# Kernel tuning notes

Measured on AMD Instinct MI355X. Metric: run time of the kernel, lower is better.

The kernel has to match this reference:

```python
import jax, jax.numpy as jnp
import numpy as np

B, S, D, H, E = 4, 1024, 1024, 16, 4
HD = D // H
FF = 4 * D
EPS = 1e-5


def _ln(x):
    # normalize only; per-expert affine applied by caller
    mu = jnp.mean(x, axis=-1, keepdims=True)
    var = jnp.mean(jnp.square(x - mu), axis=-1, keepdims=True)
    return (x - mu) * jax.lax.rsqrt(var + EPS)


def setup_inputs() -> dict:
    key = jax.random.key(0)
    ks = jax.random.split(key, 12)
    s = 0.02
    inp = {
        "x": jax.random.normal(ks[0], (B, S, D), jnp.float32),
        # attention router
        "Wr_a": jax.random.normal(ks[1], (D, E), jnp.float32) * s,
        "br_a": jnp.zeros((E,), jnp.float32),
        # per-expert attention params
        "g_a": jnp.ones((E, D), jnp.float32),
        "b_a": jnp.zeros((E, D), jnp.float32),
        "Wqkv": jax.random.normal(ks[2], (E, D, 3 * D), jnp.float32) * s,
        "bqkv": jnp.zeros((E, 3 * D), jnp.float32),
        "Wpr": jax.random.normal(ks[3], (E, D, D), jnp.float32) * s,
        "bpr": jnp.zeros((E, D), jnp.float32),
        # MLP router
        "Wr_m": jax.random.normal(ks[4], (D, E), jnp.float32) * s,
        "br_m": jnp.zeros((E,), jnp.float32),
        # per-expert MLP params
        "g_m": jnp.ones((E, D), jnp.float32),
        "b_m": jnp.zeros((E, D), jnp.float32),
        "Wfc": jax.random.normal(ks[5], (E, D, FF), jnp.float32) * s,
        "bfc": jnp.zeros((E, FF), jnp.float32),
        "Wp2": jax.random.normal(ks[6], (E, FF, D), jnp.float32) * s,
        "bp2": jnp.zeros((E, D), jnp.float32),
    }
    return inp


def _block(x, Wr_a, br_a, g_a, b_a, Wqkv, bqkv, Wpr, bpr,
           Wr_m, br_m, g_m, b_m, Wfc, bfc, Wp2, bp2):
    N = B * S
    h = x.reshape(N, D)

    # ---- MoT attention (routing_all_possible_path: dense score-weighted mix) ----
    score = jax.nn.softmax(h @ Wr_a + br_a, axis=-1)          # [N,E]
    hn = _ln(h)                                                # shared normalization
    hln = hn[None, :, :] * g_a[:, None, :] + b_a[:, None, :]  # [E,N,D]
    qkv_e = jnp.einsum('end,edf->enf', hln, Wqkv) + bqkv[:, None, :]  # [E,N,3D]
    qkv = jnp.einsum('ne,enf->nf', score, qkv_e)               # [N,3D]

    q, k, v = jnp.split(qkv.reshape(B, S, 3 * D), 3, axis=-1)
    q = q.reshape(B, S, H, HD).transpose(0, 2, 1, 3)           # [B,H,S,hd]
    k = k.reshape(B, S, H, HD).transpose(0, 2, 1, 3)
    v = v.reshape(B, S, H, HD).transpose(0, 2, 1, 3)

    aw = jnp.einsum('bhqd,bhkd->bhqk', q, k) / jnp.sqrt(jnp.float32(HD))
    causal = jnp.tril(jnp.ones((S, S), bool))
    aw = jnp.where(causal, aw, jnp.finfo(aw.dtype).min)
    p = jax.nn.softmax(aw, axis=-1)
    a = jnp.einsum('bhqk,bhkd->bhqd', p, v)                    # [B,H,S,hd]
    a = a.transpose(0, 2, 1, 3).reshape(N, D)

    attn_out = jnp.einsum('ne,nd,edf->nf', score, a, Wpr) + score @ bpr
    y = x + attn_out.reshape(B, S, D)

    # ---- MoT MLP (same dense routed-expert pattern) ----
    h2 = y.reshape(N, D)
    score2 = jax.nn.softmax(h2 @ Wr_m + br_m, axis=-1)         # [N,E]
    hn2 = _ln(h2)
    hln2 = hn2[None, :, :] * g_m[:, None, :] + b_m[:, None, :]  # [E,N,D]
    inter = jax.nn.gelu(jnp.einsum('end,edf->enf', hln2, Wfc) + bfc[:, None, :])  # [E,N,FF]
    mlp_out = jnp.einsum('ne,enf,efd->nd', score2, inter, Wp2) + score2 @ bp2
    return y + mlp_out.reshape(B, S, D)


def reference(x, Wr_a, br_a, g_a, b_a, Wqkv, bqkv, Wpr, bpr,
              Wr_m, br_m, g_m, b_m, Wfc, bfc, Wp2, bp2):
    return _block(x, Wr_a, br_a, g_a, b_a, Wqkv, bqkv, Wpr, bpr,
                  Wr_m, br_m, g_m, b_m, Wfc, bfc, Wp2, bp2)
```

## Files before the change

kernel.cpp:

```cpp
#include <hip/hip_runtime.h>
#include <hip/hip_bf16.h>

typedef __bf16 bf16x8 __attribute__((ext_vector_type(8)));
typedef float f32x4 __attribute__((ext_vector_type(4)));
typedef unsigned short u16;
typedef u16 u16x8 __attribute__((ext_vector_type(8)));
typedef u16 u16x4 __attribute__((ext_vector_type(4)));

#define B_ 4
#define S_ 1024
#define D_ 1024
#define E_ 4
#define H_ 16
#define FF_ 4096
#define N_ 4096

__device__ __forceinline__ u16 f2bf(float f) {
  __hip_bfloat16 h = __float2bfloat16(f);
  return *reinterpret_cast<u16*>(&h);
}
__device__ __forceinline__ float bf2f(u16 v) {
  return __uint_as_float(((unsigned)v) << 16);
}

#define BAR()                         \
  {                                   \
    asm volatile("" ::: "memory");    \
    __builtin_amdgcn_s_barrier();     \
    asm volatile("" ::: "memory");    \
  }

__global__ __launch_bounds__(256) void tcvt(const float* __restrict__ src,
                                            u16* __restrict__ dst, int R, int C) {
  __shared__ float t[32][33];
  long base = (long)blockIdx.z * R * C;
  src += base; dst += base;
  int r0 = blockIdx.y * 32, c0 = blockIdx.x * 32;
  int tx = threadIdx.x, ty = threadIdx.y;
#pragma unroll
  for (int i = 0; i < 4; i++)
    t[ty + i * 8][tx] = src[(long)(r0 + ty + i * 8) * C + c0 + tx];
  __syncthreads();
#pragma unroll
  for (int i = 0; i < 4; i++)
    dst[(long)(c0 + ty + i * 8) * R + r0 + tx] = f2bf(t[tx][ty + i * 8]);
}

template <int YMODE>
__global__ __launch_bounds__(256) void ln_router_expand(
    const float* __restrict__ X, const float* __restrict__ Wr, const float* __restrict__ br,
    const float* __restrict__ g, const float* __restrict__ bb,
    float* __restrict__ score_out, u16* __restrict__ Aout,
    long stride_e, long stride_n, int scale_flag,
    const float* __restrict__ score_a, const float* __restrict__ bpr,
    const u16* __restrict__ prt, float* __restrict__ ybuf) {
  int n = blockIdx.x, t = threadIdx.x;
  int lane = t & 63, wave = t >> 6;
  int d0 = t * 4;
  const float* xr = X + (long)n * D_;
  float4 xv = *reinterpret_cast<const float4*>(&xr[d0]);
  if (YMODE) {
    float4 sa4 = reinterpret_cast<const float4*>(score_a)[n];
    float sw[4] = {sa4.x, sa4.y, sa4.z, sa4.w};
    float4 b0 = *reinterpret_cast<const float4*>(&bpr[d0]);
    float4 b1 = *reinterpret_cast<const float4*>(&bpr[D_ + d0]);
    float4 b2 = *reinterpret_cast<const float4*>(&bpr[2 * D_ + d0]);
    float4 b3 = *reinterpret_cast<const float4*>(&bpr[3 * D_ + d0]);
    xv.x += sa4.x * b0.x + sa4.y * b1.x + sa4.z * b2.x + sa4.w * b3.x;
    xv.y += sa4.x * b0.y + sa4.y * b1.y + sa4.z * b2.y + sa4.w * b3.y;
    xv.z += sa4.x * b0.z + sa4.y * b1.z + sa4.z * b2.z + sa4.w * b3.z;
    xv.w += sa4.x * b0.w + sa4.y * b1.w + sa4.z * b2.w + sa4.w * b3.w;
    long idx = (long)n * D_ + d0;
#pragma unroll
    for (int zz = 0; zz < 4; zz++) {
      u16x4 pv = *reinterpret_cast<const u16x4*>(&prt[(long)zz * 4194304 + idx]);
      xv.x += sw[zz] * bf2f(pv[0]); xv.y += sw[zz] * bf2f(pv[1]);
      xv.z += sw[zz] * bf2f(pv[2]); xv.w += sw[zz] * bf2f(pv[3]);
    }
    *reinterpret_cast<float4*>(&ybuf[idx]) = xv;
  }
  float vals[6];
  vals[0] = xv.x + xv.y + xv.z + xv.w;
  vals[1] = xv.x * xv.x + xv.y * xv.y + xv.z * xv.z + xv.w * xv.w;
  {
    float4 w0 = reinterpret_cast<const float4*>(Wr)[d0];
    float4 w1 = reinterpret_cast<const float4*>(Wr)[d0 + 1];
    float4 w2 = reinterpret_cast<const float4*>(Wr)[d0 + 2];
    float4 w3 = reinterpret_cast<const float4*>(Wr)[d0 + 3];
    vals[2] = xv.x * w0.x + xv.y * w1.x + xv.z * w2.x + xv.w * w3.x;
    vals[3] = xv.x * w0.y + xv.y * w1.y + xv.z * w2.y + xv.w * w3.y;
    vals[4] = xv.x * w0.z + xv.y * w1.z + xv.z * w2.z + xv.w * w3.z;
    vals[5] = xv.x * w0.w + xv.y * w1.w + xv.z * w2.w + xv.w * w3.w;
  }
#pragma unroll
  for (int o = 1; o < 64; o <<= 1) {
#pragma unroll
    for (int j = 0; j < 6; j++) vals[j] += __shfl_xor(vals[j], o, 64);
  }
  __shared__ float red[4][6];
  if (lane == 0) {
#pragma unroll
    for (int j = 0; j < 6; j++) red[wave][j] = vals[j];
  }
  __syncthreads();
  float tot[6];
#pragma unroll
  for (int j = 0; j < 6; j++) tot[j] = red[0][j] + red[1][j] + red[2][j] + red[3][j];
  float mean = tot[0] * (1.0f / D_);
  float var = tot[1] * (1.0f / D_) - mean * mean;
  float rstd = rsqrtf(var + 1e-5f);
  float lg0 = tot[2] + br[0], lg1 = tot[3] + br[1], lg2 = tot[4] + br[2], lg3 = tot[5] + br[3];
  float mx = fmaxf(fmaxf(lg0, lg1), fmaxf(lg2, lg3));
  float e0 = __expf(lg0 - mx), e1 = __expf(lg1 - mx), e2 = __expf(lg2 - mx), e3 = __expf(lg3 - mx);
  float inv = 1.0f / (e0 + e1 + e2 + e3);
  float sc[4] = {e0 * inv, e1 * inv, e2 * inv, e3 * inv};
  if (t == 0) {
    float4 s4 = make_float4(sc[0], sc[1], sc[2], sc[3]);
    *reinterpret_cast<float4*>(&score_out[(long)n * 4]) = s4;
  }
  float4 hn;
  hn.x = (xv.x - mean) * rstd; hn.y = (xv.y - mean) * rstd;
  hn.z = (xv.z - mean) * rstd; hn.w = (xv.w - mean) * rstd;
#pragma unroll
  for (int e = 0; e < 4; e++) {
    float4 ge = *reinterpret_cast<const float4*>(&g[e * D_ + d0]);
    float4 be = *reinterpret_cast<const float4*>(&bb[e * D_ + d0]);
    float s = scale_flag ? sc[e] : 1.0f;
    u16x4 o;
    o[0] = f2bf((hn.x * ge.x + be.x) * s);
    o[1] = f2bf((hn.y * ge.y + be.y) * s);
    o[2] = f2bf((hn.z * ge.z + be.z) * s);
    o[3] = f2bf((hn.w * ge.w + be.w) * s);
    *reinterpret_cast<u16x4*>(&Aout[(long)e * stride_e + (long)n * stride_n + d0]) = o;
  }
}

template <int MODE>
__global__ __launch_bounds__(512, 2) void g8(
    const u16* __restrict__ A, const u16* __restrict__ Bt, int K, int N, int kslice,
    const float* __restrict__ score, const float* __restrict__ bias,
    u16* __restrict__ outb, int eidx, long zstride, long bz) {
  __shared__ __align__(16) u16 lds0[65536];
  const int tid = threadIdx.x;
  const int w = tid >> 6, lane = tid & 63;
  const int l15 = lane & 15, l4 = lane >> 4;
  const int wr = w >> 2, wc = w & 3;

  const int gx = gridDim.x, gy = gridDim.y;
  const int total = gx * gy * gridDim.z;
  const int flat = blockIdx.x + gx * (blockIdx.y + gy * blockIdx.z);
  const int cpx = total >> 3;
  const int nf = (flat & 7) * cpx + (flat >> 3);
  const int bxi = nf % gx;
  const int tmp = nf / gx;
  const int byi = tmp % gy;
  const int z = tmp / gy;

  const long bm = (long)byi * 256, bn = (long)bxi * 256;
  const long k0 = bz ? 0L : (long)z * kslice;
  const u16* Btz = bz ? (Bt + (long)z * bz) : Bt;
  const int nt = kslice >> 6;

  const int cp = lane & 3;
  const int sr0 = w * 32 + (lane >> 2);
  const int sr1 = sr0 + 16;
  const int cl0 = cp ^ ((sr0 >> 1) & 3);
  const int cl1 = cp ^ ((sr1 >> 1) & 3);
  const u16* gA0 = A + (bm + sr0) * (long)K + k0 + cl0 * 8;
  const u16* gA1 = A + (bm + sr1) * (long)K + k0 + cl1 * 8;
  const u16* gB0 = Btz + (bn + sr0) * (long)K + k0 + cl0 * 8;
  const u16* gB1 = Btz + (bn + sr1) * (long)K + k0 + cl1 * 8;
  const int e0 = w * 1024;
  const int e1 = w * 1024 + 512;

  const int chA = l4 ^ ((l15 >> 1) & 3);
  const int rdA = (wr * 128 + l15) * 32 + chA * 8;
  const int rdB = (wc * 64 + l15) * 32 + chA * 8;

#define GLD(gsrc, ldsoff)                                                              \
  __builtin_amdgcn_global_load_lds(                                                    \
      (const __attribute__((address_space(1))) void*)(gsrc),                           \
      (__attribute__((address_space(3))) void*)(lds0 + (ldsoff)), 16, 0, 0)

  GLD(gA0, 0 + e0);
  GLD(gA1, 0 + e1);
  GLD(gB0, 16384 + e0);
  GLD(gB1, 16384 + e1);
  GLD(gA0 + 32, 8192 + e0);
  GLD(gA1 + 32, 8192 + e1);
  GLD(gB0 + 32, 24576 + e0);
  GLD(gB1 + 32, 24576 + e1);
  if (nt > 1) {
    GLD(gA0 + 64, 32768 + e0);
    GLD(gA1 + 64, 32768 + e1);
    GLD(gB0 + 64, 32768 + 16384 + e0);
    GLD(gB1 + 64, 32768 + 16384 + e1);
    GLD(gA0 + 96, 32768 + 8192 + e0);
    GLD(gA1 + 96, 32768 + 8192 + e1);
    GLD(gB0 + 96, 32768 + 24576 + e0);
    GLD(gB1 + 96, 32768 + 24576 + e1);
    asm volatile("s_waitcnt vmcnt(8)" ::: "memory");
  } else {
    asm volatile("s_waitcnt vmcnt(0)" ::: "memory");
  }
  BAR();

  f32x4 acc[8][4] = {};
  bf16x8 aC[8], bC[4], aN[8], bN[4];

#pragma unroll
  for (int i = 0; i < 8; i++) aC[i] = *(const bf16x8*)(lds0 + rdA + i * 512);
#pragma unroll
  for (int i = 0; i < 4; i++) bC[i] = *(const bf16x8*)(lds0 + 16384 + rdB + i * 512);

  for (int t = 0; t < nt; ++t) {
    const int base = (t & 1) * 32768;
    const int nb = base ^ 32768;
    const long ko2 = (long)(t + 2) * 64;
#pragma unroll
    for (int i = 0; i < 8; i++) aN[i] = *(const bf16x8*)(lds0 + base + 8192 + rdA + i * 512);
#pragma unroll
    for (int i = 0; i < 4; i++) bN[i] = *(const bf16x8*)(lds0 + base + 24576 + rdB + i * 512);
    if (t + 2 < nt) {
      GLD(gA0 + ko2, base + e0);
      GLD(gA1 + ko2, base + e1);
      GLD(gB0 + ko2, base + 16384 + e0);
      GLD(gB1 + ko2, base + 16384 + e1);
    }
    __builtin_amdgcn_sched_barrier(0);
    __builtin_amdgcn_s_setprio(1);
#pragma unroll
    for (int mi = 0; mi < 8; mi++)
#pragma unroll
      for (int ni = 0; ni < 4; ni++)
        acc[mi][ni] = __builtin_amdgcn_mfma_f32_16x16x32_bf16(aC[mi], bC[ni], acc[mi][ni], 0, 0, 0);
    __builtin_amdgcn_s_setprio(0);
    asm volatile("s_waitcnt lgkmcnt(0)" ::: "memory");
    if (t + 1 < nt) {
      if (t + 2 < nt) {
        asm volatile("s_waitcnt vmcnt(8)" ::: "memory");
      } else {
        asm volatile("s_waitcnt vmcnt(4)" ::: "memory");
      }
    }
    BAR();
    if (t + 1 < nt) {
#pragma unroll
      for (int i = 0; i < 8; i++) aC[i] = *(const bf16x8*)(lds0 + nb + rdA + i * 512);
#pragma unroll
      for (int i = 0; i < 4; i++) bC[i] = *(const bf16x8*)(lds0 + nb + 16384 + rdB + i * 512);
    }
    if (t + 2 < nt) {
      GLD(gA0 + ko2 + 32, base + 8192 + e0);
      GLD(gA1 + ko2 + 32, base + 8192 + e1);
      GLD(gB0 + ko2 + 32, base + 24576 + e0);
      GLD(gB1 + ko2 + 32, base + 24576 + e1);
    }
    __builtin_amdgcn_sched_barrier(0);
    __builtin_amdgcn_s_setprio(1);
#pragma unroll
    for (int mi = 0; mi < 8; mi++)
#pragma unroll
      for (int ni = 0; ni < 4; ni++)
        acc[mi][ni] = __builtin_amdgcn_mfma_f32_16x16x32_bf16(aN[mi], bN[ni], acc[mi][ni], 0, 0, 0);
    __builtin_amdgcn_s_setprio(0);
    asm volatile("s_waitcnt lgkmcnt(0)" ::: "memory");
    if (t + 1 < nt) {
      if (t + 2 < nt) {
        asm volatile("s_waitcnt vmcnt(8)" ::: "memory");
      } else {
        asm volatile("s_waitcnt vmcnt(0)" ::: "memory");
      }
    }
    BAR();
  }
#undef GLD

  const long zoff = (long)z * zstride;
#pragma unroll
  for (int ni = 0; ni < 4; ni++) {
    long col = bn + wc * 64 + ni * 16 + l15;
    float b4[4];
    float bcol = 0.0f;
    if (MODE == 0) {
#pragma unroll
      for (int e = 0; e < 4; e++) b4[e] = bias[(long)e * N + col];
    } else if (MODE == 2) {
      bcol = bias[col];
    }
#pragma unroll
    for (int mi = 0; mi < 8; mi++) {
#pragma unroll
      for (int r = 0; r < 4; r++) {
        long row = bm + wr * 128 + mi * 16 + l4 * 4 + r;
        float v = acc[mi][ni][r];
        if (MODE == 0) {
          float4 s4 = reinterpret_cast<const float4*>(score)[row];
          v += s4.x * b4[0] + s4.y * b4[1] + s4.z * b4[2] + s4.w * b4[3];
          outb[row * (long)N + col] = f2bf(v);
        } else if (MODE == 2) {
          float u = v + bcol;
          float zz = 0.7978845608f * (u + 0.044715f * u * u * u);
          float tt = __expf(2.0f * zz);
          float gel = u * (1.0f - 1.0f / (tt + 1.0f));
          outb[row * (long)N + col] = f2bf(gel * score[row * 4 + eidx]);
        } else {
          outb[zoff + row * (long)N + col] = f2bf(v);
        }
      }
    }
  }
}

__global__ __launch_bounds__(256) void attn_kernel(const u16* __restrict__ qkv,
                                                   u16* __restrict__ aout) {
  __shared__ __align__(16) u16 Kt[32 * 64];
  __shared__ __align__(16) u16 VT[64 * 32];
  __shared__ __align__(16) u16 Pl[4][16 * 32];
  int tid = threadIdx.x, wave = tid >> 6, lane = tid & 63;
  int l15 = lane & 15, l4 = lane >> 4;
  int qblk = blockIdx.x, bh = blockIdx.y;
  int b = bh >> 4, h = bh & 15;
  int q0 = qblk * 64 + wave * 16;
  const long LD = 3072;

  bf16x8 qf[2];
  {
    const u16* qp = qkv + (long)(b * 1024 + q0 + l15) * LD + h * 64 + l4 * 8;
    qf[0] = *(const bf16x8*)qp;
    qf[1] = *(const bf16x8*)(qp + 32);
  }
  f32x4 acc[4] = {};
  float m_run = -1e30f, l_run = 0.0f;
  int kv_end = qblk * 64 + 64;

  for (int kv0 = 0; kv0 < kv_end; kv0 += 32) {
    {
      int r = tid >> 3, c = (tid & 7) * 8;
      const u16* kp = qkv + (long)(b * 1024 + kv0 + r) * LD + 1024 + h * 64 + c;
      *(u16x8*)&Kt[r * 64 + c] = *(const u16x8*)kp;
      u16x8 vv = *(const u16x8*)(kp + 1024);
#pragma unroll
      for (int j = 0; j < 8; j++) VT[(c + j) * 32 + r] = vv[j];
    }
    __syncthreads();
    if (kv0 < q0 + 16) {
      float p[8];
      float pmax = -1e30f;
      int qg = q0 + l15;
#pragma unroll
      for (int ks = 0; ks < 2; ks++) {
        f32x4 st = {};
#pragma unroll
        for (int kc = 0; kc < 2; kc++) {
          bf16x8 kf = *(const bf16x8*)&Kt[(ks * 16 + l15) * 64 + kc * 32 + l4 * 8];
          st = __builtin_amdgcn_mfma_f32_16x16x32_bf16(kf, qf[kc], st, 0, 0, 0);
        }
#pragma unroll
        for (int r = 0; r < 4; r++) {
          int kvg = kv0 + ks * 16 + l4 * 4 + r;
          float v = st[r] * 0.125f;
          if (kvg > qg) v = -1e30f;
          p[ks * 4 + r] = v;
          pmax = fmaxf(pmax, v);
        }
      }
      pmax = fmaxf(pmax, __shfl_xor(pmax, 16, 64));
      pmax = fmaxf(pmax, __shfl_xor(pmax, 32, 64));
      float m_new = fmaxf(m_run, pmax);
      float alpha = __expf(m_run - m_new);
      float rsum = 0.f;
#pragma unroll
      for (int i = 0; i < 8; i++) {
        p[i] = __expf(p[i] - m_new);
        rsum += p[i];
      }
      rsum += __shfl_xor(rsum, 16, 64);
      rsum += __shfl_xor(rsum, 32, 64);
      l_run = l_run * alpha + rsum;
      m_run = m_new;
      float af4[4];
#pragma unroll
      for (int r = 0; r < 4; r++) af4[r] = __shfl(alpha, l4 * 4 + r, 64);
#pragma unroll
      for (int i = 0; i < 4; i++) {
#pragma unroll
        for (int r = 0; r < 4; r++) acc[i][r] *= af4[r];
      }
      u16* pw = &Pl[wave][0];
#pragma unroll
      for (int i = 0; i < 8; i++) {
        int ks = i >> 2, r = i & 3;
        pw[l15 * 32 + ks * 16 + l4 * 4 + r] = f2bf(p[i]);
      }
      bf16x8 pa = *(const bf16x8*)&pw[l15 * 32 + l4 * 8];
#pragma unroll
      for (int i = 0; i < 4; i++) {
        bf16x8 vf = *(const bf16x8*)&VT[(i * 16 + l15) * 32 + l4 * 8];
        acc[i] = __builtin_amdgcn_mfma_f32_16x16x32_bf16(pa, vf, acc[i], 0, 0, 0);
      }
    }
    __syncthreads();
  }

  float linv[4];
#pragma unroll
  for (int r = 0; r < 4; r++) {
    float lv = __shfl(l_run, l4 * 4 + r, 64);
    linv[r] = 1.0f / lv;
  }
#pragma unroll
  for (int r = 0; r < 4; r++) {
    int q = l4 * 4 + r;
    long nrow = (long)b * 1024 + q0 + q;
#pragma unroll
    for (int i = 0; i < 4; i++) {
      int d = h * 64 + i * 16 + l15;
      aout[nrow * 1024 + d] = f2bf(acc[i][r] * linv[r]);
    }
  }
}

template <int FIRST>
__global__ __launch_bounds__(256) void accum_out(const float* __restrict__ ybuf,
                                                 const float* __restrict__ score_m,
                                                 const float* __restrict__ bp2,
                                                 const u16* __restrict__ p2t,
                                                 float* __restrict__ out) {
  int n = blockIdx.x, t = threadIdx.x;
  int d0 = t * 4;
  long idx = (long)n * D_ + d0;
  float4 v;
  if (FIRST) {
    float4 s4 = reinterpret_cast<const float4*>(score_m)[n];
    float4 b0 = *reinterpret_cast<const float4*>(&bp2[d0]);
    float4 b1 = *reinterpret_cast<const float4*>(&bp2[D_ + d0]);
    float4 b2 = *reinterpret_cast<const float4*>(&bp2[2 * D_ + d0]);
    float4 b3 = *reinterpret_cast<const float4*>(&bp2[3 * D_ + d0]);
    v = *reinterpret_cast<const float4*>(&ybuf[idx]);
    v.x += s4.x * b0.x + s4.y * b1.x + s4.z * b2.x + s4.w * b3.x;
    v.y += s4.x * b0.y + s4.y * b1.y + s4.z * b2.y + s4.w * b3.y;
    v.z += s4.x * b0.z + s4.y * b1.z + s4.z * b2.z + s4.w * b3.z;
    v.w += s4.x * b0.w + s4.y * b1.w + s4.z * b2.w + s4.w * b3.w;
  } else {
    v = *reinterpret_cast<const float4*>(&out[idx]);
  }
#pragma unroll
  for (int zz = 0; zz < 4; zz++) {
    u16x4 pv = *reinterpret_cast<const u16x4*>(&p2t[(long)zz * 4194304 + idx]);
    v.x += bf2f(pv[0]); v.y += bf2f(pv[1]); v.z += bf2f(pv[2]); v.w += bf2f(pv[3]);
  }
  *reinterpret_cast<float4*>(&out[idx]) = v;
}

extern "C" void kernel_launch(void* const* d_in, const int* in_sizes, int n_in, void* d_out,
                              int out_size, void* d_ws, size_t ws_size, hipStream_t stream) {
  (void)in_sizes; (void)n_in; (void)out_size; (void)ws_size;
  const float* x    = (const float*)d_in[0];
  const float* Wr_a = (const float*)d_in[1];
  const float* br_a = (const float*)d_in[2];
  const float* g_a  = (const float*)d_in[3];
  const float* b_a  = (const float*)d_in[4];
  const float* Wqkv = (const float*)d_in[5];
  const float* bqkv = (const float*)d_in[6];
  const float* Wpr  = (const float*)d_in[7];
  const float* bpr  = (const float*)d_in[8];
  const float* Wr_m = (const float*)d_in[9];
  const float* br_m = (const float*)d_in[10];
  const float* g_m  = (const float*)d_in[11];
  const float* b_m  = (const float*)d_in[12];
  const float* Wfc  = (const float*)d_in[13];
  const float* bfc  = (const float*)d_in[14];
  const float* Wp2  = (const float*)d_in[15];
  const float* bp2  = (const float*)d_in[16];
  float* out = (float*)d_out;

  char* ws = (char*)d_ws;
  const size_t R1 = 0;
  const size_t R2 = 33554432;
  const size_t R3 = 67108864;
  const size_t R4 = 100663296;
  const size_t R5 = 134217728;
  const size_t R6 = 167772160;
  const size_t R7 = 184549376;
  u16* wt_qkv  = (u16*)(ws + R1);
  u16* wt_pr   = (u16*)(ws + R1);
  u16* wt_fc   = (u16*)(ws + R1);
  u16* wt_p2   = (u16*)(ws + R2);
  u16* A_a     = (u16*)(ws + R2);
  u16* qkvb    = (u16*)(ws + R3);
  u16* A_fc    = (u16*)(ws + R3);
  u16* abuf    = (u16*)(ws + R4);
  u16* inter   = (u16*)(ws + R4);
  u16* prt     = (u16*)(ws + R5);
  u16* p2t     = (u16*)(ws + R5);
  float* ybuf  = (float*)(ws + R6);
  float* score_a = (float*)(ws + R7);
  float* score_m = (float*)(ws + R7 + 65536);

  dim3 tb(32, 8);
  tcvt<<<dim3(3072 / 32, 4096 / 32, 1), tb, 0, stream>>>(Wqkv, wt_qkv, 4096, 3072);
  ln_router_expand<0><<<N_, 256, 0, stream>>>(x, Wr_a, br_a, g_a, b_a, score_a, A_a,
                                              (long)1024, (long)4096, 1,
                                              nullptr, nullptr, nullptr, nullptr);
  g8<0><<<dim3(3072 / 256, 4096 / 256, 1), 512, 0, stream>>>(
      A_a, wt_qkv, 4096, 3072, 4096, score_a, bqkv, qkvb, 0, 0L, 0L);
  attn_kernel<<<dim3(S_ / 64, B_ * H_), 256, 0, stream>>>(qkvb, abuf);
  tcvt<<<dim3(1024 / 32, 1024 / 32, 4), tb, 0, stream>>>(Wpr, wt_pr, 1024, 1024);
  g8<4><<<dim3(1024 / 256, 4096 / 256, 4), 512, 0, stream>>>(
      abuf, wt_pr, 1024, 1024, 1024, nullptr, nullptr, prt, 0,
      (long)4096 * 1024, (long)1024 * 1024);

  tcvt<<<dim3(4096 / 32, 1024 / 32, 4), tb, 0, stream>>>(Wfc, wt_fc, 1024, 4096);
  tcvt<<<dim3(1024 / 32, 4096 / 32, 4), tb, 0, stream>>>(Wp2, wt_p2, 4096, 1024);
  ln_router_expand<1><<<N_, 256, 0, stream>>>(x, Wr_m, br_m, g_m, b_m,
                                              score_m, A_fc, (long)N_ * 1024, (long)1024, 0,
                                              score_a, bpr, prt, ybuf);
  for (int e = 0; e < 4; e++) {
    g8<2><<<dim3(4096 / 256, 4096 / 256, 1), 512, 0, stream>>>(
        A_fc + (size_t)e * N_ * 1024, wt_fc + (size_t)e * 4096 * 1024, 1024, 4096, 1024,
        score_m, bfc + e * 4096, inter, e, 0L, 0L);
    g8<4><<<dim3(1024 / 256, 4096 / 256, 4), 512, 0, stream>>>(
        inter, wt_p2 + (size_t)e * 1024 * 4096, 4096, 1024, 1024, nullptr, nullptr,
        p2t, 0, (long)4096 * 1024, 0L);
    if (e == 0) {
      accum_out<1><<<N_, 256, 0, stream>>>(ybuf, score_m, bp2, p2t, out);
    } else {
      accum_out<0><<<N_, 256, 0, stream>>>(nullptr, nullptr, nullptr, p2t, out);
    }
  }
}
```

Measured before the change: 791.8 us.

## Split GEMM main loop into four MFMA clusters with interleaved staggered prefetch

```diff
diff --git a/kernel.cpp b/kernel.cpp
--- a/kernel.cpp
+++ b/kernel.cpp
@@ -184,97 +184,95 @@
 
   GLD(gA0, 0 + e0);
   GLD(gA1, 0 + e1);
+  GLD(gA0 + 32, 8192 + e0);
+  GLD(gA1 + 32, 8192 + e1);
   GLD(gB0, 16384 + e0);
   GLD(gB1, 16384 + e1);
-  GLD(gA0 + 32, 8192 + e0);
-  GLD(gA1 + 32, 8192 + e1);
   GLD(gB0 + 32, 24576 + e0);
   GLD(gB1 + 32, 24576 + e1);
   if (nt > 1) {
-    GLD(gA0 + 64, 32768 + e0);
-    GLD(gA1 + 64, 32768 + e1);
     GLD(gB0 + 64, 32768 + 16384 + e0);
     GLD(gB1 + 64, 32768 + 16384 + e1);
-    GLD(gA0 + 96, 32768 + 8192 + e0);
-    GLD(gA1 + 96, 32768 + 8192 + e1);
+    GLD(gA0 + 64, 32768 + 0 + e0);
+    GLD(gA1 + 64, 32768 + 0 + e1);
     GLD(gB0 + 96, 32768 + 24576 + e0);
     GLD(gB1 + 96, 32768 + 24576 + e1);
-    asm volatile("s_waitcnt vmcnt(8)" ::: "memory");
+    asm volatile("s_waitcnt vmcnt(6)" ::: "memory");
   } else {
     asm volatile("s_waitcnt vmcnt(0)" ::: "memory");
   }
   BAR();
 
   f32x4 acc[8][4] = {};
-  bf16x8 aC[8], bC[4], aN[8], bN[4];
-
-#pragma unroll
-  for (int i = 0; i < 8; i++) aC[i] = *(const bf16x8*)(lds0 + rdA + i * 512);
-#pragma unroll
-  for (int i = 0; i < 4; i++) bC[i] = *(const bf16x8*)(lds0 + 16384 + rdB + i * 512);
+  bf16x8 a[4], b[4];
+
+#define MFMA_CLUSTER(mibase)                                                           \
+  asm volatile("s_waitcnt lgkmcnt(0)" ::: "memory");                                   \
+  __builtin_amdgcn_sched_barrier(0);                                                   \
+  __builtin_amdgcn_s_setprio(1);                                                       \
+  _Pragma("unroll")                                                                    \
+  for (int mi = 0; mi < 4; mi++)                                                       \
+    _Pragma("unroll")                                                                  \
+    for (int ni = 0; ni < 4; ni++)                                                     \
+      acc[(mibase) + mi][ni] =                                                         \
+          __builtin_amdgcn_mfma_f32_16x16x32_bf16(a[mi], b[ni], acc[(mibase) + mi][ni],\
+                                                  0, 0, 0);                            \
+  __builtin_amdgcn_s_setprio(0);
 
   for (int t = 0; t < nt; ++t) {
-    const int base = (t & 1) * 32768;
-    const int nb = base ^ 32768;
+    const int buf = (t & 1) * 32768;
+    const int nxt = buf ^ 32768;
+    const long ko1 = (long)(t + 1) * 64;
     const long ko2 = (long)(t + 2) * 64;
 #pragma unroll
-    for (int i = 0; i < 8; i++) aN[i] = *(const bf16x8*)(lds0 + base + 8192 + rdA + i * 512);
-#pragma unroll
-    for (int i = 0; i < 4; i++) bN[i] = *(const bf16x8*)(lds0 + base + 24576 + rdB + i * 512);
+    for (int i = 0; i < 4; i++) a[i] = *(const bf16x8*)(lds0 + buf + rdA + i * 512);
+#pragma unroll
+    for (int i = 0; i < 4; i++) b[i] = *(const bf16x8*)(lds0 + buf + 16384 + rdB + i * 512);
+    if (t + 1 < nt) {
+      GLD(gA0 + ko1 + 32, nxt + 8192 + e0);
+      GLD(gA1 + ko1 + 32, nxt + 8192 + e1);
+    }
+    __builtin_amdgcn_s_barrier();
+    MFMA_CLUSTER(0);
+    __builtin_amdgcn_s_barrier();
+#pragma unroll
+    for (int i = 0; i < 4; i++) a[i] = *(const bf16x8*)(lds0 + buf + rdA + (4 + i) * 512);
     if (t + 2 < nt) {
-      GLD(gA0 + ko2, base + e0);
-      GLD(gA1 + ko2, base + e1);
-      GLD(gB0 + ko2, base + 16384 + e0);
-      GLD(gB1 + ko2, base + 16384 + e1);
-    }
-    __builtin_amdgcn_sched_barrier(0);
-    __builtin_amdgcn_s_setprio(1);
-#pragma unroll
-    for (int mi = 0; mi < 8; mi++)
-#pragma unroll
-      for (int ni = 0; ni < 4; ni++)
-        acc[mi][ni] = __builtin_amdgcn_mfma_f32_16x16x32_bf16(aC[mi], bC[ni], acc[mi][ni], 0, 0, 0);
-    __builtin_amdgcn_s_setprio(0);
-    asm volatile("s_waitcnt lgkmcnt(0)" ::: "memory");
-    if (t + 1 < nt) {
-      if (t + 2 < nt) {
-        asm volatile("s_waitcnt vmcnt(8)" ::: "memory");
-      } else {
-        asm volatile("s_waitcnt vmcnt(4)" ::: "memory");
-      }
+      GLD(gB0 + ko2, buf + 16384 + e0);
+      GLD(gB1 + ko2, buf + 16384 + e1);
+    }
+    __builtin_amdgcn_s_barrier();
+    MFMA_CLUSTER(4);
+    __builtin_amdgcn_s_barrier();
+#pragma unroll
+    for (int i = 0; i < 4; i++) a[i] = *(const bf16x8*)(lds0 + buf + 8192 + rdA + i * 512);
+#pragma unroll
+    for (int i = 0; i < 4; i++) b[i] = *(const bf16x8*)(lds0 + buf + 24576 + rdB + i * 512);
+    if (t + 2 < nt) {
+      GLD(gA0 + ko2, buf + 0 + e0);
+      GLD(gA1 + ko2, buf + 0 + e1);
+    }
+    __builtin_amdgcn_s_barrier();
+    MFMA_CLUSTER(0);
+    __builtin_amdgcn_s_barrier();
+#pragma unroll
+    for (int i = 0; i < 4; i++)
+      a[i] = *(const bf16x8*)(lds0 + buf + 8192 + rdA + (4 + i) * 512);
+    if (t + 2 < nt) {
+      GLD(gB0 + ko2 + 32, buf + 24576 + e0);
+      GLD(gB1 + ko2 + 32, buf + 24576 + e1);
+    }
+    __builtin_amdgcn_s_barrier();
+    MFMA_CLUSTER(4);
+    if (t + 2 < nt) {
+      asm volatile("s_waitcnt vmcnt(6)" ::: "memory");
+    } else if (t + 1 < nt) {
+      asm volatile("s_waitcnt vmcnt(0)" ::: "memory");
     }
     BAR();
-    if (t + 1 < nt) {
-#pragma unroll
-      for (int i = 0; i < 8; i++) aC[i] = *(const bf16x8*)(lds0 + nb + rdA + i * 512);
-#pragma unroll
-      for (int i = 0; i < 4; i++) bC[i] = *(const bf16x8*)(lds0 + nb + 16384 + rdB + i * 512);
-    }
-    if (t + 2 < nt) {
-      GLD(gA0 + ko2 + 32, base + 8192 + e0);
-      GLD(gA1 + ko2 + 32, base + 8192 + e1);
-      GLD(gB0 + ko2 + 32, base + 24576 + e0);
-      GLD(gB1 + ko2 + 32, base + 24576 + e1);
-    }
-    __builtin_amdgcn_sched_barrier(0);
-    __builtin_amdgcn_s_setprio(1);
-#pragma unroll
-    for (int mi = 0; mi < 8; mi++)
-#pragma unroll
-      for (int ni = 0; ni < 4; ni++)
-        acc[mi][ni] = __builtin_amdgcn_mfma_f32_16x16x32_bf16(aN[mi], bN[ni], acc[mi][ni], 0, 0, 0);
-    __builtin_amdgcn_s_setprio(0);
-    asm volatile("s_waitcnt lgkmcnt(0)" ::: "memory");
-    if (t + 1 < nt) {
-      if (t + 2 < nt) {
-        asm volatile("s_waitcnt vmcnt(8)" ::: "memory");
-      } else {
-        asm volatile("s_waitcnt vmcnt(0)" ::: "memory");
-      }
-    }
-    BAR();
   }
 #undef GLD
+#undef MFMA_CLUSTER
 
   const long zoff = (long)z * zstride;
 #pragma unroll
```

Result: no change. 798.7 us (+0.9%).

## Fold MLP layernorm affine into FC weights and bias, share normalized input

Applied to the files above, without the earlier changes.

```diff
diff --git a/kernel.cpp b/kernel.cpp
--- a/kernel.cpp
+++ b/kernel.cpp
@@ -46,7 +46,41 @@
     dst[(long)(c0 + ty + i * 8) * R + r0 + tx] = f2bf(t[tx][ty + i * 8]);
 }
 
-template <int YMODE>
+__global__ __launch_bounds__(256) void tcvtg(const float* __restrict__ src,
+                                             u16* __restrict__ dst, int R, int C,
+                                             const float* __restrict__ gv) {
+  __shared__ float t[32][33];
+  long base = (long)blockIdx.z * R * C;
+  src += base; dst += base;
+  gv += (long)blockIdx.z * R;
+  int r0 = blockIdx.y * 32, c0 = blockIdx.x * 32;
+  int tx = threadIdx.x, ty = threadIdx.y;
+#pragma unroll
+  for (int i = 0; i < 4; i++) {
+    int r = r0 + ty + i * 8;
+    t[ty + i * 8][tx] = gv[r] * src[(long)r * C + c0 + tx];
+  }
+  __syncthreads();
+#pragma unroll
+  for (int i = 0; i < 4; i++)
+    dst[(long)(c0 + ty + i * 8) * R + r0 + tx] = f2bf(t[tx][ty + i * 8]);
+}
+
+__global__ __launch_bounds__(256) void cbias(const float* __restrict__ W,
+                                             const float* __restrict__ bvec,
+                                             const float* __restrict__ bias0,
+                                             float* __restrict__ outb, int Dd, int FF) {
+  int e = blockIdx.y;
+  int f = blockIdx.x * 256 + threadIdx.x;
+  const float* We = W + (size_t)e * Dd * FF + f;
+  const float* be = bvec + (size_t)e * Dd;
+  float acc = 0.f;
+#pragma unroll 4
+  for (int d = 0; d < Dd; d++) acc += be[d] * We[(size_t)d * FF];
+  outb[(size_t)e * FF + f] = bias0[(size_t)e * FF + f] + acc;
+}
+
+template <int YMODE, int EXPAND>
 __global__ __launch_bounds__(256) void ln_router_expand(
     const float* __restrict__ X, const float* __restrict__ Wr, const float* __restrict__ br,
     const float* __restrict__ g, const float* __restrict__ bb,
@@ -121,17 +155,23 @@
   float4 hn;
   hn.x = (xv.x - mean) * rstd; hn.y = (xv.y - mean) * rstd;
   hn.z = (xv.z - mean) * rstd; hn.w = (xv.w - mean) * rstd;
-#pragma unroll
-  for (int e = 0; e < 4; e++) {
-    float4 ge = *reinterpret_cast<const float4*>(&g[e * D_ + d0]);
-    float4 be = *reinterpret_cast<const float4*>(&bb[e * D_ + d0]);
-    float s = scale_flag ? sc[e] : 1.0f;
+  if (EXPAND) {
+#pragma unroll
+    for (int e = 0; e < 4; e++) {
+      float4 ge = *reinterpret_cast<const float4*>(&g[e * D_ + d0]);
+      float4 be = *reinterpret_cast<const float4*>(&bb[e * D_ + d0]);
+      float s = scale_flag ? sc[e] : 1.0f;
+      u16x4 o;
+      o[0] = f2bf((hn.x * ge.x + be.x) * s);
+      o[1] = f2bf((hn.y * ge.y + be.y) * s);
+      o[2] = f2bf((hn.z * ge.z + be.z) * s);
+      o[3] = f2bf((hn.w * ge.w + be.w) * s);
+      *reinterpret_cast<u16x4*>(&Aout[(long)e * stride_e + (long)n * stride_n + d0]) = o;
+    }
+  } else {
     u16x4 o;
-    o[0] = f2bf((hn.x * ge.x + be.x) * s);
-    o[1] = f2bf((hn.y * ge.y + be.y) * s);
-    o[2] = f2bf((hn.z * ge.z + be.z) * s);
-    o[3] = f2bf((hn.w * ge.w + be.w) * s);
-    *reinterpret_cast<u16x4*>(&Aout[(long)e * stride_e + (long)n * stride_n + d0]) = o;
+    o[0] = f2bf(hn.x); o[1] = f2bf(hn.y); o[2] = f2bf(hn.z); o[3] = f2bf(hn.w);
+    *reinterpret_cast<u16x4*>(&Aout[(long)n * 1024 + d0]) = o;
   }
 }
 
@@ -227,7 +267,6 @@
       GLD(gB0 + ko2, base + 16384 + e0);
       GLD(gB1 + ko2, base + 16384 + e1);
     }
-    __builtin_amdgcn_sched_barrier(0);
     __builtin_amdgcn_s_setprio(1);
 #pragma unroll
     for (int mi = 0; mi < 8; mi++)
@@ -256,7 +295,6 @@
       GLD(gB0 + ko2 + 32, base + 24576 + e0);
       GLD(gB1 + ko2 + 32, base + 24576 + e1);
     }
-    __builtin_amdgcn_sched_barrier(0);
     __builtin_amdgcn_s_setprio(1);
 #pragma unroll
     for (int mi = 0; mi < 8; mi++)
@@ -484,25 +522,26 @@
   const size_t R6 = 167772160;
   const size_t R7 = 184549376;
   u16* wt_qkv  = (u16*)(ws + R1);
-  u16* wt_pr   = (u16*)(ws + R1);
   u16* wt_fc   = (u16*)(ws + R1);
+  u16* A_a     = (u16*)(ws + R2);
   u16* wt_p2   = (u16*)(ws + R2);
-  u16* A_a     = (u16*)(ws + R2);
   u16* qkvb    = (u16*)(ws + R3);
-  u16* A_fc    = (u16*)(ws + R3);
-  u16* abuf    = (u16*)(ws + R4);
+  u16* hn_buf  = (u16*)(ws + R3);
+  u16* wt_pr   = (u16*)(ws + R4);
+  u16* abuf    = (u16*)(ws + R4 + (size_t)8 * 1024 * 1024);
   u16* inter   = (u16*)(ws + R4);
   u16* prt     = (u16*)(ws + R5);
   u16* p2t     = (u16*)(ws + R5);
   float* ybuf  = (float*)(ws + R6);
   float* score_a = (float*)(ws + R7);
   float* score_m = (float*)(ws + R7 + 65536);
+  float* Cbf     = (float*)(ws + R7 + 131072);
 
   dim3 tb(32, 8);
   tcvt<<<dim3(3072 / 32, 4096 / 32, 1), tb, 0, stream>>>(Wqkv, wt_qkv, 4096, 3072);
-  ln_router_expand<0><<<N_, 256, 0, stream>>>(x, Wr_a, br_a, g_a, b_a, score_a, A_a,
-                                              (long)1024, (long)4096, 1,
-                                              nullptr, nullptr, nullptr, nullptr);
+  ln_router_expand<0, 1><<<N_, 256, 0, stream>>>(x, Wr_a, br_a, g_a, b_a, score_a, A_a,
+                                                 (long)1024, (long)4096, 1,
+                                                 nullptr, nullptr, nullptr, nullptr);
   g8<0><<<dim3(3072 / 256, 4096 / 256, 1), 512, 0, stream>>>(
       A_a, wt_qkv, 4096, 3072, 4096, score_a, bqkv, qkvb, 0, 0L, 0L);
   attn_kernel<<<dim3(S_ / 64, B_ * H_), 256, 0, stream>>>(qkvb, abuf);
@@ -511,15 +550,16 @@
       abuf, wt_pr, 1024, 1024, 1024, nullptr, nullptr, prt, 0,
       (long)4096 * 1024, (long)1024 * 1024);
 
-  tcvt<<<dim3(4096 / 32, 1024 / 32, 4), tb, 0, stream>>>(Wfc, wt_fc, 1024, 4096);
+  tcvtg<<<dim3(4096 / 32, 1024 / 32, 4), tb, 0, stream>>>(Wfc, wt_fc, 1024, 4096, g_m);
+  cbias<<<dim3(4096 / 256, 4), 256, 0, stream>>>(Wfc, b_m, bfc, Cbf, 1024, 4096);
   tcvt<<<dim3(1024 / 32, 4096 / 32, 4), tb, 0, stream>>>(Wp2, wt_p2, 4096, 1024);
-  ln_router_expand<1><<<N_, 256, 0, stream>>>(x, Wr_m, br_m, g_m, b_m,
-                                              score_m, A_fc, (long)N_ * 1024, (long)1024, 0,
-                                              score_a, bpr, prt, ybuf);
+  ln_router_expand<1, 0><<<N_, 256, 0, stream>>>(x, Wr_m, br_m, nullptr, nullptr,
+                                                 score_m, hn_buf, 0L, (long)1024, 0,
+                                                 score_a, bpr, prt, ybuf);
   for (int e = 0; e < 4; e++) {
     g8<2><<<dim3(4096 / 256, 4096 / 256, 1), 512, 0, stream>>>(
-        A_fc + (size_t)e * N_ * 1024, wt_fc + (size_t)e * 4096 * 1024, 1024, 4096, 1024,
-        score_m, bfc + e * 4096, inter, e, 0L, 0L);
+        hn_buf, wt_fc + (size_t)e * 4096 * 1024, 1024, 4096, 1024,
+        score_m, Cbf + e * 4096, inter, e, 0L, 0L);
     g8<4><<<dim3(1024 / 256, 4096 / 256, 4), 512, 0, stream>>>(
         inter, wt_p2 + (size_t)e * 1024 * 4096, 4096, 1024, 1024, nullptr, nullptr,
         p2t, 0, (long)4096 * 1024, 0L);
```

Result: slower. 865.9 us (+9.4%).

## Split fused QKV GEMM into per-expert batched GEMMs plus a score-mix kernel

Applied to the files above, without the earlier changes.

```diff
diff --git a/kernel.cpp b/kernel.cpp
--- a/kernel.cpp
+++ b/kernel.cpp
@@ -46,7 +46,7 @@
     dst[(long)(c0 + ty + i * 8) * R + r0 + tx] = f2bf(t[tx][ty + i * 8]);
 }
 
-template <int YMODE>
+template <int YMODE, int EXPAND>
 __global__ __launch_bounds__(256) void ln_router_expand(
     const float* __restrict__ X, const float* __restrict__ Wr, const float* __restrict__ br,
     const float* __restrict__ g, const float* __restrict__ bb,
@@ -121,25 +121,52 @@
   float4 hn;
   hn.x = (xv.x - mean) * rstd; hn.y = (xv.y - mean) * rstd;
   hn.z = (xv.z - mean) * rstd; hn.w = (xv.w - mean) * rstd;
+  if (EXPAND) {
+#pragma unroll
+    for (int e = 0; e < 4; e++) {
+      float4 ge = *reinterpret_cast<const float4*>(&g[e * D_ + d0]);
+      float4 be = *reinterpret_cast<const float4*>(&bb[e * D_ + d0]);
+      float s = scale_flag ? sc[e] : 1.0f;
+      u16x4 o;
+      o[0] = f2bf((hn.x * ge.x + be.x) * s);
+      o[1] = f2bf((hn.y * ge.y + be.y) * s);
+      o[2] = f2bf((hn.z * ge.z + be.z) * s);
+      o[3] = f2bf((hn.w * ge.w + be.w) * s);
+      *reinterpret_cast<u16x4*>(&Aout[(long)e * stride_e + (long)n * stride_n + d0]) = o;
+    }
+  } else {
+    u16x4 o;
+    o[0] = f2bf(hn.x); o[1] = f2bf(hn.y); o[2] = f2bf(hn.z); o[3] = f2bf(hn.w);
+    *reinterpret_cast<u16x4*>(&Aout[(long)n * 1024 + d0]) = o;
+  }
+}
+
+__global__ __launch_bounds__(256) void mixq(const u16* __restrict__ qp,
+                                            const float* __restrict__ score_a,
+                                            const float* __restrict__ bqkv,
+                                            u16* __restrict__ qkvb) {
+  int c = blockIdx.x * 256 + threadIdx.x;
+  int n = c / 384, f0 = (c % 384) * 8;
+  float4 s4 = reinterpret_cast<const float4*>(score_a)[n];
+  float sw[4] = {s4.x, s4.y, s4.z, s4.w};
+  float acc[8] = {};
 #pragma unroll
   for (int e = 0; e < 4; e++) {
-    float4 ge = *reinterpret_cast<const float4*>(&g[e * D_ + d0]);
-    float4 be = *reinterpret_cast<const float4*>(&bb[e * D_ + d0]);
-    float s = scale_flag ? sc[e] : 1.0f;
-    u16x4 o;
-    o[0] = f2bf((hn.x * ge.x + be.x) * s);
-    o[1] = f2bf((hn.y * ge.y + be.y) * s);
-    o[2] = f2bf((hn.z * ge.z + be.z) * s);
-    o[3] = f2bf((hn.w * ge.w + be.w) * s);
-    *reinterpret_cast<u16x4*>(&Aout[(long)e * stride_e + (long)n * stride_n + d0]) = o;
-  }
+    u16x8 pv = *reinterpret_cast<const u16x8*>(&qp[(long)e * 12582912 + (long)n * 3072 + f0]);
+#pragma unroll
+    for (int j = 0; j < 8; j++) acc[j] += bf2f(pv[j]) + sw[e] * bqkv[e * 3072 + f0 + j];
+  }
+  u16x8 o;
+#pragma unroll
+  for (int j = 0; j < 8; j++) o[j] = f2bf(acc[j]);
+  *reinterpret_cast<u16x8*>(&qkvb[(long)n * 3072 + f0]) = o;
 }
 
 template <int MODE>
 __global__ __launch_bounds__(512, 2) void g8(
     const u16* __restrict__ A, const u16* __restrict__ Bt, int K, int N, int kslice,
     const float* __restrict__ score, const float* __restrict__ bias,
-    u16* __restrict__ outb, int eidx, long zstride, long bz) {
+    u16* __restrict__ outb, int eidx, long zstride, long az, long bz) {
   __shared__ __align__(16) u16 lds0[65536];
   const int tid = threadIdx.x;
   const int w = tid >> 6, lane = tid & 63;
@@ -158,6 +185,7 @@
 
   const long bm = (long)byi * 256, bn = (long)bxi * 256;
   const long k0 = bz ? 0L : (long)z * kslice;
+  const u16* Az = bz ? (A + (long)z * az) : A;
   const u16* Btz = bz ? (Bt + (long)z * bz) : Bt;
   const int nt = kslice >> 6;
 
@@ -166,8 +194,8 @@
   const int sr1 = sr0 + 16;
   const int cl0 = cp ^ ((sr0 >> 1) & 3);
   const int cl1 = cp ^ ((sr1 >> 1) & 3);
-  const u16* gA0 = A + (bm + sr0) * (long)K + k0 + cl0 * 8;
-  const u16* gA1 = A + (bm + sr1) * (long)K + k0 + cl1 * 8;
+  const u16* gA0 = Az + (bm + sr0) * (long)K + k0 + cl0 * 8;
+  const u16* gA1 = Az + (bm + sr1) * (long)K + k0 + cl1 * 8;
   const u16* gB0 = Btz + (bn + sr0) * (long)K + k0 + cl0 * 8;
   const u16* gB1 = Btz + (bn + sr1) * (long)K + k0 + cl1 * 8;
   const int e0 = w * 1024;
@@ -227,7 +255,6 @@
       GLD(gB0 + ko2, base + 16384 + e0);
       GLD(gB1 + ko2, base + 16384 + e1);
     }
-    __builtin_amdgcn_sched_barrier(0);
     __builtin_amdgcn_s_setprio(1);
 #pragma unroll
     for (int mi = 0; mi < 8; mi++)
@@ -256,7 +283,6 @@
       GLD(gB0 + ko2 + 32, base + 24576 + e0);
       GLD(gB1 + ko2 + 32, base + 24576 + e1);
     }
-    __builtin_amdgcn_sched_barrier(0);
     __builtin_amdgcn_s_setprio(1);
 #pragma unroll
     for (int mi = 0; mi < 8; mi++)
@@ -280,25 +306,14 @@
 #pragma unroll
   for (int ni = 0; ni < 4; ni++) {
     long col = bn + wc * 64 + ni * 16 + l15;
-    float b4[4];
-    float bcol = 0.0f;
-    if (MODE == 0) {
-#pragma unroll
-      for (int e = 0; e < 4; e++) b4[e] = bias[(long)e * N + col];
-    } else if (MODE == 2) {
-      bcol = bias[col];
-    }
+    float bcol = (MODE == 2) ? bias[col] : 0.0f;
 #pragma unroll
     for (int mi = 0; mi < 8; mi++) {
 #pragma unroll
       for (int r = 0; r < 4; r++) {
         long row = bm + wr * 128 + mi * 16 + l4 * 4 + r;
         float v = acc[mi][ni][r];
-        if (MODE == 0) {
-          float4 s4 = reinterpret_cast<const float4*>(score)[row];
-          v += s4.x * b4[0] + s4.y * b4[1] + s4.z * b4[2] + s4.w * b4[3];
-          outb[row * (long)N + col] = f2bf(v);
-        } else if (MODE == 2) {
+        if (MODE == 2) {
           float u = v + bcol;
           float zz = 0.7978845608f * (u + 0.044715f * u * u * u);
           float tt = __expf(2.0f * zz);
@@ -476,53 +491,49 @@
   float* out = (float*)d_out;
 
   char* ws = (char*)d_ws;
-  const size_t R1 = 0;
-  const size_t R2 = 33554432;
-  const size_t R3 = 67108864;
-  const size_t R4 = 100663296;
-  const size_t R5 = 134217728;
-  const size_t R6 = 167772160;
-  const size_t R7 = 184549376;
-  u16* wt_qkv  = (u16*)(ws + R1);
-  u16* wt_pr   = (u16*)(ws + R1);
-  u16* wt_fc   = (u16*)(ws + R1);
-  u16* wt_p2   = (u16*)(ws + R2);
-  u16* A_a     = (u16*)(ws + R2);
-  u16* qkvb    = (u16*)(ws + R3);
-  u16* A_fc    = (u16*)(ws + R3);
-  u16* abuf    = (u16*)(ws + R4);
-  u16* inter   = (u16*)(ws + R4);
-  u16* prt     = (u16*)(ws + R5);
-  u16* p2t     = (u16*)(ws + R5);
-  float* ybuf  = (float*)(ws + R6);
-  float* score_a = (float*)(ws + R7);
-  float* score_m = (float*)(ws + R7 + 65536);
+  u16* wt_q   = (u16*)(ws + 0);
+  u16* wt_fc  = (u16*)(ws + 0);
+  u16* A_a    = (u16*)(ws + 33554432);
+  u16* wt_p2  = (u16*)(ws + 33554432);
+  u16* qp     = (u16*)(ws + 67108864);
+  u16* A_fc   = (u16*)(ws + 67108864);
+  u16* inter  = (u16*)(ws + 100663296);
+  u16* p2t    = (u16*)(ws + 134217728);
+  u16* qkvb   = (u16*)(ws + 167772160);
+  u16* prt    = (u16*)(ws + 167772160);
+  u16* abuf   = (u16*)(ws + 201326592);
+  float* ybuf = (float*)(ws + 209715200);
+  float* score_a = (float*)(ws + 226492416);
+  float* score_m = (float*)(ws + 226492416 + 65536);
 
   dim3 tb(32, 8);
-  tcvt<<<dim3(3072 / 32, 4096 / 32, 1), tb, 0, stream>>>(Wqkv, wt_qkv, 4096, 3072);
-  ln_router_expand<0><<<N_, 256, 0, stream>>>(x, Wr_a, br_a, g_a, b_a, score_a, A_a,
-                                              (long)1024, (long)4096, 1,
-                                              nullptr, nullptr, nullptr, nullptr);
-  g8<0><<<dim3(3072 / 256, 4096 / 256, 1), 512, 0, stream>>>(
-      A_a, wt_qkv, 4096, 3072, 4096, score_a, bqkv, qkvb, 0, 0L, 0L);
+  tcvt<<<dim3(3072 / 32, 1024 / 32, 4), tb, 0, stream>>>(Wqkv, wt_q, 1024, 3072);
+  ln_router_expand<0, 1><<<N_, 256, 0, stream>>>(x, Wr_a, br_a, g_a, b_a, score_a, A_a,
+                                                 (long)4096 * 1024, (long)1024, 1,
+                                                 nullptr, nullptr, nullptr, nullptr);
+  g8<4><<<dim3(3072 / 256, 4096 / 256, 4), 512, 0, stream>>>(
+      A_a, wt_q, 1024, 3072, 1024, nullptr, nullptr, qp, 0,
+      (long)4096 * 3072, (long)4096 * 1024, (long)3072 * 1024);
+  mixq<<<(4096 * 384) / 256, 256, 0, stream>>>(qp, score_a, bqkv, qkvb);
   attn_kernel<<<dim3(S_ / 64, B_ * H_), 256, 0, stream>>>(qkvb, abuf);
+  u16* wt_pr = A_a;
   tcvt<<<dim3(1024 / 32, 1024 / 32, 4), tb, 0, stream>>>(Wpr, wt_pr, 1024, 1024);
   g8<4><<<dim3(1024 / 256, 4096 / 256, 4), 512, 0, stream>>>(
       abuf, wt_pr, 1024, 1024, 1024, nullptr, nullptr, prt, 0,
-      (long)4096 * 1024, (long)1024 * 1024);
+      (long)4096 * 1024, 0L, (long)1024 * 1024);
 
   tcvt<<<dim3(4096 / 32, 1024 / 32, 4), tb, 0, stream>>>(Wfc, wt_fc, 1024, 4096);
   tcvt<<<dim3(1024 / 32, 4096 / 32, 4), tb, 0, stream>>>(Wp2, wt_p2, 4096, 1024);
-  ln_router_expand<1><<<N_, 256, 0, stream>>>(x, Wr_m, br_m, g_m, b_m,
-                                              score_m, A_fc, (long)N_ * 1024, (long)1024, 0,
-                                              score_a, bpr, prt, ybuf);
+  ln_router_expand<1, 1><<<N_, 256, 0, stream>>>(x, Wr_m, br_m, g_m, b_m,
+                                                 score_m, A_fc, (long)N_ * 1024, (long)1024,
+                                                 0, score_a, bpr, prt, ybuf);
   for (int e = 0; e < 4; e++) {
     g8<2><<<dim3(4096 / 256, 4096 / 256, 1), 512, 0, stream>>>(
         A_fc + (size_t)e * N_ * 1024, wt_fc + (size_t)e * 4096 * 1024, 1024, 4096, 1024,
-        score_m, bfc + e * 4096, inter, e, 0L, 0L);
+        score_m, bfc + e * 4096, inter, e, 0L, 0L, 0L);
     g8<4><<<dim3(1024 / 256, 4096 / 256, 4), 512, 0, stream>>>(
         inter, wt_p2 + (size_t)e * 1024 * 4096, 4096, 1024, 1024, nullptr, nullptr,
-        p2t, 0, (long)4096 * 1024, 0L);
+        p2t, 0, (long)4096 * 1024, 0L, 0L);
     if (e == 0) {
       accum_out<1><<<N_, 256, 0, stream>>>(ybuf, score_m, bp2, p2t, out);
     } else {
```

Result: no change. 783.7 us (-1.0%).
